# Optimization experiments

Measured on AMD Instinct MI355X. Metric: run time of the kernel, lower is better.

## Reference

```python
import jax, jax.numpy as jnp
import numpy as np

N = 100_000   # nodes (patches)
E = 500_000   # directed edges (kNN, k=5)
F_IN, NHID, GDIM, NCLS = 512, 128, 32, 3
RATIO = 0.2

def _k(n):
    return int(np.ceil(RATIO * n))

K1, K2, K3 = _k(N), _k(_k(N)), _k(_k(_k(N)))


def setup_inputs() -> dict:
    key = jax.random.key(0)
    ks = jax.random.split(key, 20)
    def w(k, shape):
        fan_in = shape[0]
        return jax.random.normal(k, shape, jnp.float32) / np.sqrt(fan_in)
    return {
        "x": jax.random.normal(ks[0], (N, F_IN), jnp.float32),
        "edge_index": jax.random.randint(ks[1], (2, E), 0, N, jnp.int32),
        # SAGEConv1 (lin_l on aggregated msgs w/ bias, lin_r on root w/o bias)
        "w1l": w(ks[2], (F_IN, NHID)), "b1l": jnp.zeros((NHID,), jnp.float32),
        "w1r": w(ks[3], (F_IN, NHID)),
        # SAGPooling1 score GNN = GCNConv(nhid, 1)
        "g1w": w(ks[4], (NHID, 1)), "g1b": jnp.zeros((1,), jnp.float32),
        "w2l": w(ks[5], (NHID, NHID)), "b2l": jnp.zeros((NHID,), jnp.float32),
        "w2r": w(ks[6], (NHID, NHID)),
        "g2w": w(ks[7], (NHID, 1)), "g2b": jnp.zeros((1,), jnp.float32),
        "w3l": w(ks[8], (NHID, NHID)), "b3l": jnp.zeros((NHID,), jnp.float32),
        "w3r": w(ks[9], (NHID, NHID)),
        "g3w": w(ks[10], (NHID, 1)), "g3b": jnp.zeros((1,), jnp.float32),
        "lw1": w(ks[11], (2 * NHID, NHID)), "lb1": jnp.zeros((NHID,), jnp.float32),
        "lw2": w(ks[12], (NHID, GDIM)), "lb2": jnp.zeros((GDIM,), jnp.float32),
        "lw3": w(ks[13], (GDIM, NCLS)), "lb3": jnp.zeros((NCLS,), jnp.float32),
    }


def sage_conv(x, src, dst, ev, Wl, bl, Wr, n):
    """PyG SAGEConv: lin_l(mean_{j->i} x_j) + lin_r(x_i); ev is float edge-valid mask."""
    msg = x[src] * ev[:, None]                      # [E, F] gather
    agg = jax.ops.segment_sum(msg, dst, num_segments=n)
    cnt = jax.ops.segment_sum(ev, dst, num_segments=n)
    mean = agg / jnp.maximum(cnt, 1.0)[:, None]
    return mean @ Wl + bl + x @ Wr


def gcn_score(x, src, dst, ev, W, b, n):
    """GCNConv(nhid,1) with self-loops and symmetric norm -> per-node score [n]."""
    xw = x @ W                                       # [n, 1]
    deg = jax.ops.segment_sum(ev, dst, num_segments=n) + 1.0  # self-loop
    dis = jax.lax.rsqrt(deg)
    norm = dis[src] * dis[dst] * ev                  # [E]
    agg = jax.ops.segment_sum(xw[src] * norm[:, None], dst, num_segments=n)
    agg = agg + xw * (dis * dis)[:, None]            # self-loop term
    return (agg + b)[:, 0]


def sag_pool(x, src, dst, ev, W, b, n, k):
    """SAGPooling: top-k by GCN score, x' = x[perm] * tanh(score[perm]); relabel/mask edges."""
    score = gcn_score(x, src, dst, ev, W, b, n)
    topv, perm = jax.lax.top_k(score, k)
    xk = x[perm] * jnp.tanh(topv)[:, None]
    rank = jnp.full((n,), -1, jnp.int32).at[perm].set(jnp.arange(k, dtype=jnp.int32))
    ns, nd = rank[src], rank[dst]
    nev = ev * ((ns >= 0) & (nd >= 0)).astype(x.dtype)
    return xk, jnp.maximum(ns, 0), jnp.maximum(nd, 0), nev


def reference(x, edge_index, w1l, b1l, w1r, g1w, g1b, w2l, b2l, w2r, g2w, g2b,
              w3l, b3l, w3r, g3w, g3b, lw1, lb1, lw2, lb2, lw3, lb3):
    src, dst = edge_index[0], edge_index[1]
    ev = jnp.ones((src.shape[0],), x.dtype)

    h = jax.nn.relu(sage_conv(x, src, dst, ev, w1l, b1l, w1r, N))
    h, src, dst, ev = sag_pool(h, src, dst, ev, g1w, g1b, N, K1)
    x1 = jnp.concatenate([h.max(axis=0), h.mean(axis=0)])[None]   # [1, 2*nhid]

    h = jax.nn.relu(sage_conv(h, src, dst, ev, w2l, b2l, w2r, K1))
    h, src, dst, ev = sag_pool(h, src, dst, ev, g2w, g2b, K1, K2)
    x2 = jnp.concatenate([h.max(axis=0), h.mean(axis=0)])[None]

    h = jax.nn.relu(sage_conv(h, src, dst, ev, w3l, b3l, w3r, K2))
    h, src, dst, ev = sag_pool(h, src, dst, ev, g3w, g3b, K2, K3)
    x3 = jnp.concatenate([h.max(axis=0), h.mean(axis=0)])[None]

    g = x1 + x2 + x3
    g = jax.nn.relu(g @ lw1 + lb1)          # dropout is identity in eval
    features = jax.nn.relu(g @ lw2 + lb2)   # [1, grph_dim]
    out = features @ lw3 + lb3              # [1, num_classes], act=None
    return features, out
```

## Files before the change

### kernel.cpp

```cpp
#include <hip/hip_runtime.h>
#include <hip/hip_bf16.h>
#include <cstdint>
#include <cstddef>

#define N_NODES 100000
#define N_EDGES 500000
#define F_IN    512
#define NHID    128
#define KP1     20000
#define KP2     4000
#define KP3     800
#define GDIM    32
#define NCLS    3
#define HISTB   128
#define RDB     64
#define RELB    768

typedef __attribute__((ext_vector_type(8))) short bf16x8;
typedef __attribute__((ext_vector_type(4))) float f32x4;

static __device__ __forceinline__ unsigned enc_f(float f) {
  unsigned u = __float_as_uint(f);
  return (u & 0x80000000u) ? ~u : (u | 0x80000000u);
}
static __device__ __forceinline__ float dec_f(unsigned u) {
  unsigned v = (u & 0x80000000u) ? (u & 0x7FFFFFFFu) : ~u;
  return __uint_as_float(v);
}
static __device__ __forceinline__ unsigned short f2bf(float f) {
  unsigned u = __float_as_uint(f);
  return (unsigned short)((u + 0x7FFFu + ((u >> 16) & 1u)) >> 16);
}
static __device__ __forceinline__ unsigned pk2(float a, float b) {
  return (unsigned)f2bf(a) | ((unsigned)f2bf(b) << 16);
}
static __device__ __forceinline__ float bf2f(unsigned short v) {
  return __uint_as_float(((unsigned)v) << 16);
}

static __device__ __forceinline__ void hist_tail(int hb, int t, int nthreads,
                                                 const int* __restrict__ dst,
                                                 const int* __restrict__ ev,
                                                 int* __restrict__ cnt) {
  for (int e = hb * nthreads + t; e < N_EDGES; e += HISTB * nthreads) {
    if (ev && !ev[e]) continue;
    atomicAdd(cnt + dst[e], 1);
  }
}

__global__ __launch_bounds__(256) void wt_prep(const float* __restrict__ w1l,
                                               const float* __restrict__ w1r,
                                               const float* __restrict__ w2l,
                                               const float* __restrict__ w2r,
                                               const float* __restrict__ w3l,
                                               const float* __restrict__ w3r,
                                               unsigned short* __restrict__ Wt,
                                               unsigned short* __restrict__ Wt2,
                                               unsigned short* __restrict__ Wt3,
                                               int* __restrict__ cnt0,
                                               unsigned* __restrict__ hist) {
  __shared__ unsigned short T[128][130];
  int blk = blockIdx.x;
  int t = threadIdx.x;
  if (blk == 0) hist[t] = 0u;
  for (int i = blk * 256 + t; i < N_NODES; i += (int)gridDim.x * 256) cnt0[i] = 0;

  const float* W;
  unsigned short* Wo;
  int mat, k0, KW;
  if (blk < 8) {
    mat = blk >> 2; k0 = (blk & 3) * 128; KW = 512;
    W = mat ? w1r : w1l; Wo = Wt;
  } else if (blk < 10) {
    mat = blk - 8; k0 = 0; KW = 128;
    W = mat ? w2r : w2l; Wo = Wt2;
  } else {
    mat = blk - 10; k0 = 0; KW = 128;
    W = mat ? w3r : w3l; Wo = Wt3;
  }
  for (int q = 0; q < 64; ++q) {
    int idx = q * 256 + t;
    int r = idx >> 7, c = idx & 127;
    T[r][c] = f2bf(W[(size_t)(k0 + r) * 128 + c]);
  }
  __syncthreads();
  int nn = t & 127;
  int kc = (t >> 7) * 64;
  for (int j8 = 0; j8 < 8; ++j8) {
    uint4 w;
    int kb = kc + j8 * 8;
    w.x = (unsigned)T[kb + 0][nn] | ((unsigned)T[kb + 1][nn] << 16);
    w.y = (unsigned)T[kb + 2][nn] | ((unsigned)T[kb + 3][nn] << 16);
    w.z = (unsigned)T[kb + 4][nn] | ((unsigned)T[kb + 5][nn] << 16);
    w.w = (unsigned)T[kb + 6][nn] | ((unsigned)T[kb + 7][nn] << 16);
    *reinterpret_cast<uint4*>(Wo + ((size_t)(mat * 128 + nn) * KW + k0 + kb)) = w;
  }
}

__global__ __launch_bounds__(512) void gemm_mfma(const void* __restrict__ Ain, int aBf16,
                                                 const unsigned short* __restrict__ Wt,
                                                 unsigned short* __restrict__ O1b,
                                                 unsigned short* __restrict__ Gb,
                                                 int n, int K, int nbA,
                                                 const int* __restrict__ edst,
                                                 const int* __restrict__ eev,
                                                 int* __restrict__ cnt,
                                                 const unsigned short* __restrict__ Hprev,
                                                 int kprev,
                                                 unsigned* __restrict__ maxaccP,
                                                 float* __restrict__ sumaccP) {
  __shared__ unsigned short Alds[128 * 64];
  __shared__ float red[4][128];
  const int t = threadIdx.x;
  if ((int)blockIdx.x >= nbA + HISTB) {
    int hb = blockIdx.x - nbA - HISTB;
    int f = t & 127, rg = t >> 7;
    float m = -INFINITY, s = 0.f;
    for (int r = hb * 4 + rg; r < kprev; r += RDB * 4) {
      float v = bf2f(Hprev[(size_t)r * 128 + f]);
      m = fmaxf(m, v); s += v;
    }
    red[rg][f] = m;
    __syncthreads();
    if (t < 128) {
      float mm = fmaxf(fmaxf(red[0][t], red[1][t]), fmaxf(red[2][t], red[3][t]));
      atomicMax(maxaccP + t, enc_f(mm));
    }
    __syncthreads();
    red[rg][f] = s;
    __syncthreads();
    if (t < 128) {
      float ss = red[0][t] + red[1][t] + red[2][t] + red[3][t];
      atomicAdd(sumaccP + t, ss);
    }
    return;
  }
  if ((int)blockIdx.x >= nbA) {
    hist_tail(blockIdx.x - nbA, t, 512, edst, eev, cnt);
    return;
  }
  const int wave = t >> 6;
  const int lane = t & 63;
  const int wr = wave >> 2;
  const int wc = wave & 3;
  const int l15 = lane & 15, l4 = lane >> 4;
  const int bm = blockIdx.x * 128;
  f32x4 zero = {0.f, 0.f, 0.f, 0.f};
  f32x4 acc[4][4];
#pragma unroll
  for (int i = 0; i < 4; ++i)
#pragma unroll
    for (int j = 0; j < 4; ++j) acc[i][j] = zero;

  const int sr = t >> 2;
  const int skc = (t & 3) * 16;
  const int sgr = bm + sr;
  const float* apf = (const float*)Ain + (size_t)sgr * K + skc;
  const unsigned short* apb = (const unsigned short*)Ain + (size_t)sgr * K + skc;
  const unsigned sbase = sr * 128 + skc * 2;
  const unsigned ssw = (sr & 7) << 4;

  for (int k0 = 0; k0 < K; k0 += 64) {
    __syncthreads();
    if (aBf16) {
      uint4 w0 = make_uint4(0u, 0u, 0u, 0u), w1 = make_uint4(0u, 0u, 0u, 0u);
      if (sgr < n) {
        w0 = *reinterpret_cast<const uint4*>(apb + k0);
        w1 = *reinterpret_cast<const uint4*>(apb + k0 + 8);
      }
      *reinterpret_cast<uint4*>((char*)Alds + (sbase ^ ssw)) = w0;
      *reinterpret_cast<uint4*>((char*)Alds + ((sbase + 16) ^ ssw)) = w1;
    } else {
      float4 v0, v1, v2, v3;
      if (sgr < n) {
        v0 = *reinterpret_cast<const float4*>(apf + k0);
        v1 = *reinterpret_cast<const float4*>(apf + k0 + 4);
        v2 = *reinterpret_cast<const float4*>(apf + k0 + 8);
        v3 = *reinterpret_cast<const float4*>(apf + k0 + 12);
      } else {
        v0 = v1 = v2 = v3 = make_float4(0.f, 0.f, 0.f, 0.f);
      }
      uint4 w0, w1;
      w0.x = pk2(v0.x, v0.y); w0.y = pk2(v0.z, v0.w);
      w0.z = pk2(v1.x, v1.y); w0.w = pk2(v1.z, v1.w);
      w1.x = pk2(v2.x, v2.y); w1.y = pk2(v2.z, v2.w);
      w1.z = pk2(v3.x, v3.y); w1.w = pk2(v3.z, v3.w);
      *reinterpret_cast<uint4*>((char*)Alds + (sbase ^ ssw)) = w0;
      *reinterpret_cast<uint4*>((char*)Alds + ((sbase + 16) ^ ssw)) = w1;
    }
    __syncthreads();
#pragma unroll
    for (int kk = 0; kk < 2; ++kk) {
      bf16x8 af[4], bfr[4];
#pragma unroll
      for (int fr = 0; fr < 4; ++fr) {
        int row = wr * 64 + fr * 16 + l15;
        unsigned ba = (unsigned)(row * 128 + kk * 64 + l4 * 16) ^ ((unsigned)(row & 7) << 4);
        af[fr] = *reinterpret_cast<const bf16x8*>((const char*)Alds + ba);
      }
#pragma unroll
      for (int fn = 0; fn < 4; ++fn) {
        int col = wc * 64 + fn * 16 + l15;
        bfr[fn] = *reinterpret_cast<const bf16x8*>(Wt + ((size_t)col * K + k0 + kk * 32 + l4 * 8));
      }
#pragma unroll
      for (int fr = 0; fr < 4; ++fr)
#pragma unroll
        for (int fn = 0; fn < 4; ++fn)
          acc[fr][fn] = __builtin_amdgcn_mfma_f32_16x16x32_bf16(af[fr], bfr[fn], acc[fr][fn], 0, 0, 0);
    }
  }

#pragma unroll
  for (int fr = 0; fr < 4; ++fr) {
#pragma unroll
    for (int fn = 0; fn < 4; ++fn) {
      int colg = wc * 64 + fn * 16 + l15;
      int col = colg & 127;
      int row0 = bm + wr * 64 + fr * 16 + l4 * 4;
#pragma unroll
      for (int r2 = 0; r2 < 4; ++r2) {
        int gr = row0 + r2;
        if (gr < n) {
          unsigned short bv = f2bf(acc[fr][fn][r2]);
          if (colg < 128) O1b[(size_t)gr * 128 + col] = bv;
          else            Gb [(size_t)gr * 128 + col] = bv;
        }
      }
    }
  }
}

__global__ void scan1(const int* __restrict__ cnt, int n,
                      int* __restrict__ incl, int* __restrict__ bsum) {
  __shared__ int sh[256];
  int t = threadIdx.x, i = blockIdx.x * 256 + t;
  int v = (i < n) ? cnt[i] : 0;
  sh[t] = v; __syncthreads();
  for (int o = 1; o < 256; o <<= 1) {
    int a = (t >= o) ? sh[t - o] : 0;
    __syncthreads(); sh[t] += a; __syncthreads();
  }
  if (i < n) incl[i] = sh[t];
  if (t == 255) bsum[blockIdx.x] = sh[255];
}

__global__ void scan2(int* __restrict__ bsum, int nb) {
  __shared__ int sh[512];
  int t = threadIdx.x;
  int v = (t < nb) ? bsum[t] : 0;
  sh[t] = v; __syncthreads();
  for (int o = 1; o < 512; o <<= 1) {
    int a = (t >= o) ? sh[t - o] : 0;
    __syncthreads(); sh[t] += a; __syncthreads();
  }
  if (t < nb) bsum[t] = sh[t] - v;
}

__global__ void scan3(const int* __restrict__ cnt, const int* __restrict__ incl,
                      const int* __restrict__ bsum, int n,
                      int* __restrict__ rowstart, int* __restrict__ ptr,
                      int* __restrict__ cnt_next, int n_next) {
  int i = blockIdx.x * 256 + threadIdx.x;
  if (i < n_next) cnt_next[i] = 0;
  if (i >= n) return;
  int excl = incl[i] - cnt[i] + bsum[blockIdx.x];
  rowstart[i] = excl; ptr[i] = excl;
  if (i == n - 1) rowstart[n] = excl + cnt[i];
}

__global__ __launch_bounds__(1024) void csr_scan_one(const int* __restrict__ cnt, int n,
                                                     int* __restrict__ rowstart,
                                                     int* __restrict__ ptr,
                                                     int* __restrict__ cnt_next, int n_next) {
  __shared__ int sg[1024];
  const int t = threadIdx.x;
  for (int i = t; i < n_next; i += 1024) cnt_next[i] = 0;
  const int chunk = (n + 1023) >> 10;
  const int i0 = t * chunk;
  const int i1 = (i0 + chunk < n) ? i0 + chunk : n;
  int c = 0;
  for (int i = i0; i < i1; ++i) c += cnt[i];
  sg[t] = c;
  __syncthreads();
  for (int o = 1; o < 1024; o <<= 1) {
    int a = (t >= o) ? sg[t - o] : 0;
    __syncthreads();
    sg[t] += a;
    __syncthreads();
  }
  int excl = sg[t] - c;
  for (int i = i0; i < i1; ++i) {
    rowstart[i] = excl; ptr[i] = excl;
    excl += cnt[i];
  }
  if (t == 1023) rowstart[n] = sg[1023];
}

__global__ void scatter_csr(const int* __restrict__ src, const int* __restrict__ dst,
                            const int* __restrict__ ev, int* __restrict__ ptr,
                            int* __restrict__ csr_src) {
  int e = blockIdx.x * 256 + threadIdx.x;
  if (e >= N_EDGES) return;
  if (ev && !ev[e]) return;
  int p = atomicAdd(ptr + dst[e], 1);
  csr_src[p] = src[e];
}

__global__ void segsort(const int* __restrict__ rowstart, int* __restrict__ csr, int n) {
  int i = blockIdx.x * 256 + threadIdx.x;
  if (i >= n) return;
  int b = rowstart[i], e = rowstart[i + 1];
  for (int j = b + 1; j < e; ++j) {
    int v = csr[j], k = j - 1;
    while (k >= b && csr[k] > v) { csr[k + 1] = csr[k]; --k; }
    csr[k + 1] = v;
  }
}

__global__ void agg_fin(const unsigned short* __restrict__ X1b, const int* __restrict__ rowstart,
                        const int* __restrict__ csr, const float* __restrict__ bias,
                        const float* __restrict__ gw,
                        unsigned short* __restrict__ Gb, float* __restrict__ xw, int n) {
  int wid = (blockIdx.x * 256 + threadIdx.x) >> 6;
  if (wid >= n) return;
  int lane = threadIdx.x & 63;
  int b = rowstart[wid], e = rowstart[wid + 1];
  float sx = 0.f, sy = 0.f;
  int p = b;
  for (; p + 3 < e; p += 4) {
    int s0 = csr[p], s1 = csr[p + 1], s2 = csr[p + 2], s3 = csr[p + 3];
    unsigned v0 = *reinterpret_cast<const unsigned*>(X1b + (size_t)s0 * 128 + lane * 2);
    unsigned v1 = *reinterpret_cast<const unsigned*>(X1b + (size_t)s1 * 128 + lane * 2);
    unsigned v2 = *reinterpret_cast<const unsigned*>(X1b + (size_t)s2 * 128 + lane * 2);
    unsigned v3 = *reinterpret_cast<const unsigned*>(X1b + (size_t)s3 * 128 + lane * 2);
    sx += bf2f((unsigned short)(v0 & 0xFFFFu)); sy += bf2f((unsigned short)(v0 >> 16));
    sx += bf2f((unsigned short)(v1 & 0xFFFFu)); sy += bf2f((unsigned short)(v1 >> 16));
    sx += bf2f((unsigned short)(v2 & 0xFFFFu)); sy += bf2f((unsigned short)(v2 >> 16));
    sx += bf2f((unsigned short)(v3 & 0xFFFFu)); sy += bf2f((unsigned short)(v3 >> 16));
  }
  for (; p < e; ++p) {
    int s0 = csr[p];
    unsigned v0 = *reinterpret_cast<const unsigned*>(X1b + (size_t)s0 * 128 + lane * 2);
    sx += bf2f((unsigned short)(v0 & 0xFFFFu));
    sy += bf2f((unsigned short)(v0 >> 16));
  }
  int c = e - b; if (c < 1) c = 1;
  float inv = 1.f / (float)c;
  float2 bi = *reinterpret_cast<const float2*>(bias + lane * 2);
  unsigned gv = *reinterpret_cast<const unsigned*>(Gb + (size_t)wid * 128 + lane * 2);
  float gx = bf2f((unsigned short)(gv & 0xFFFFu));
  float gy = bf2f((unsigned short)(gv >> 16));
  float2 o = make_float2(fmaxf(sx * inv + bi.x + gx, 0.f),
                         fmaxf(sy * inv + bi.y + gy, 0.f));
  *reinterpret_cast<unsigned*>(Gb + (size_t)wid * 128 + lane * 2) = pk2(o.x, o.y);
  float2 gwv = *reinterpret_cast<const float2*>(gw + lane * 2);
  float s = o.x * gwv.x + o.y * gwv.y;
  for (int off = 32; off; off >>= 1) s += __shfl_down(s, off);
  if (lane == 0) xw[wid] = s;
}

__global__ void gcn_score_csr(const float* __restrict__ xw, const int* __restrict__ rowstart,
                              const int* __restrict__ csr, const int* __restrict__ cnt,
                              const float* __restrict__ gb,
                              float* __restrict__ score, unsigned* __restrict__ keys, int n,
                              unsigned* __restrict__ state, int kout) {
  int i = blockIdx.x * 256 + threadIdx.x;
  if (i == 0) { state[0] = 0u; state[1] = (unsigned)kout; }
  if (i >= n) return;
  int b = rowstart[i], e = rowstart[i + 1];
  float di = rsqrtf((float)(e - b) + 1.f);
  float s = 0.f;
  int p = b;
  for (; p + 3 < e; p += 4) {
    int s0 = csr[p], s1 = csr[p + 1], s2 = csr[p + 2], s3 = csr[p + 3];
    float x0 = xw[s0], x1 = xw[s1], x2 = xw[s2], x3 = xw[s3];
    float c0 = (float)cnt[s0], c1 = (float)cnt[s1];
    float c2 = (float)cnt[s2], c3 = (float)cnt[s3];
    s += x0 * rsqrtf(c0 + 1.f);
    s += x1 * rsqrtf(c1 + 1.f);
    s += x2 * rsqrtf(c2 + 1.f);
    s += x3 * rsqrtf(c3 + 1.f);
  }
  for (; p < e; ++p) {
    int s0 = csr[p];
    s += xw[s0] * rsqrtf((float)cnt[s0] + 1.f);
  }
  float sc = s * di + xw[i] * di * di + gb[0];
  score[i] = sc;
  keys[i] = enc_f(sc);
}

__global__ void topk_hist(const unsigned* __restrict__ keys, int n,
                          const unsigned* __restrict__ state, unsigned mask, int shift,
                          unsigned* __restrict__ hist) {
  __shared__ unsigned h[256];
  int t = threadIdx.x;
  h[t] = 0u;
  __syncthreads();
  unsigned pref = state[0];
  for (int i = blockIdx.x * 256 + t; i < n; i += gridDim.x * 256) {
    unsigned k = keys[i];
    if ((k & mask) == pref) atomicAdd(&h[(k >> shift) & 0xFFu], 1u);
  }
  __syncthreads();
  unsigned hv = h[t];
  if (hv) atomicAdd(&hist[t], hv);
}

__global__ void topk_pick(unsigned* state, unsigned* hist, int shift) {
  __shared__ unsigned h[256], a[256];
  int t = threadIdx.x;
  unsigned hv = hist[t];
  hist[t] = 0;
  h[t] = hv;
  __syncthreads();
  a[t] = h[255 - t];
  __syncthreads();
  for (int o = 1; o < 256; o <<= 1) {
    unsigned v = (t >= o) ? a[t - o] : 0u;
    __syncthreads();
    a[t] += v;
    __syncthreads();
  }
  unsigned krem = state[1];
  unsigned Sb  = a[255 - t];
  unsigned Sb1 = (t == 255) ? 0u : a[255 - (t + 1)];
  if (Sb >= krem && Sb1 < krem) {
    state[0] |= ((unsigned)t) << shift;
    state[1] = krem - Sb1;
  }
}

__global__ void scanA(const unsigned* __restrict__ keys, int n,
                      const unsigned* __restrict__ state,
                      unsigned* __restrict__ pgt, unsigned* __restrict__ peq) {
  __shared__ unsigned sg[256], se[256];
  int t = threadIdx.x;
  int i = blockIdx.x * 256 + t;
  unsigned kth = state[0];
  unsigned g = 0, e = 0;
  if (i < n) { unsigned k = keys[i]; g = (k > kth); e = (k == kth); }
  sg[t] = g; se[t] = e;
  __syncthreads();
  for (int s = 128; s; s >>= 1) {
    if (t < s) { sg[t] += sg[t + s]; se[t] += se[t + s]; }
    __syncthreads();
  }
  if (t == 0) { pgt[blockIdx.x] = sg[0]; peq[blockIdx.x] = se[0]; }
}

__global__ void scanB(unsigned* pgt, unsigned* peq, int nb,
                      unsigned* __restrict__ maxacc, float* __restrict__ sumacc) {
  __shared__ unsigned a[512], b[512];
  int t = threadIdx.x;
  if (t < 128) { maxacc[t] = 0u; sumacc[t] = 0.f; }
  unsigned og = (t < nb) ? pgt[t] : 0u;
  unsigned oe = (t < nb) ? peq[t] : 0u;
  a[t] = og; b[t] = oe;
  __syncthreads();
  for (int o = 1; o < 512; o <<= 1) {
    unsigned av = (t >= o) ? a[t - o] : 0u;
    unsigned bv = (t >= o) ? b[t - o] : 0u;
    __syncthreads();
    a[t] += av; b[t] += bv;
    __syncthreads();
  }
  if (t < nb) { pgt[t] = a[t] - og; peq[t] = b[t] - oe; }
}

__global__ void scanC(const unsigned* __restrict__ keys, int n,
                      const unsigned* __restrict__ state,
                      const unsigned* __restrict__ pgt, const unsigned* __restrict__ peq,
                      int K, int* __restrict__ rank) {
  __shared__ unsigned sg[256], se[256];
  int t = threadIdx.x;
  int i = blockIdx.x * 256 + t;
  unsigned kth = state[0], krem = state[1];
  unsigned g = 0, e = 0;
  if (i < n) { unsigned k = keys[i]; g = (k > kth); e = (k == kth); }
  sg[t] = g; se[t] = e;
  __syncthreads();
  for (int o = 1; o < 256; o <<= 1) {
    unsigned av = (t >= o) ? sg[t - o] : 0u;
    unsigned bv = (t >= o) ? se[t - o] : 0u;
    __syncthreads();
    sg[t] += av; se[t] += bv;
    __syncthreads();
  }
  if (i < n) {
    int r = -1;
    unsigned n_gt = (unsigned)K - krem;
    if (g) r = (int)(pgt[blockIdx.x] + sg[t] - 1);
    else if (e) {
      unsigned pe = peq[blockIdx.x] + se[t] - 1;
      if (pe < krem) r = (int)(n_gt + pe);
    }
    rank[i] = r;
  }
}

__global__ __launch_bounds__(1024) void select_one(const unsigned* __restrict__ keys, int n,
                                                   int K, int* __restrict__ rank,
                                                   unsigned* __restrict__ maxacc,
                                                   float* __restrict__ sumacc) {
  __shared__ unsigned h[256], a[256];
  __shared__ unsigned sg[1024], se[1024];
  __shared__ unsigned s_pref, s_krem;
  const int t = threadIdx.x;
  if (t < 128) { maxacc[t] = 0u; sumacc[t] = 0.f; }
  if (t == 0) { s_pref = 0u; s_krem = (unsigned)K; }
  __syncthreads();

#pragma unroll
  for (int p = 0; p < 4; ++p) {
    const int shift = 24 - 8 * p;
    const unsigned mask = (p == 0) ? 0u : (0xFFFFFFFFu << (shift + 8));
    if (t < 256) h[t] = 0u;
    __syncthreads();
    unsigned pref = s_pref;
    for (int i = t; i < n; i += 1024) {
      unsigned k = keys[i];
      if ((k & mask) == pref) atomicAdd(&h[(k >> shift) & 0xFFu], 1u);
    }
    __syncthreads();
    if (t < 256) a[t] = h[255 - t];
    __syncthreads();
    for (int o = 1; o < 256; o <<= 1) {
      unsigned v = (t >= o && t < 256) ? a[t - o] : 0u;
      __syncthreads();
      if (t < 256) a[t] += v;
      __syncthreads();
    }
    unsigned krem = s_krem;
    __syncthreads();
    if (t < 256) {
      unsigned Sb  = a[255 - t];
      unsigned Sb1 = (t == 255) ? 0u : a[255 - (t + 1)];
      if (Sb >= krem && Sb1 < krem) {
        s_pref |= ((unsigned)t) << shift;
        s_krem = krem - Sb1;
      }
    }
    __syncthreads();
  }

  const unsigned kth = s_pref;
  const unsigned krem = s_krem;
  const unsigned n_gt = (unsigned)K - krem;
  const int chunk = (n + 1023) >> 10;
  const int i0 = t * chunk;
  const int i1 = (i0 + chunk < n) ? i0 + chunk : n;
  unsigned cg = 0, ce = 0;
  for (int i = i0; i < i1; ++i) {
    unsigned k = keys[i];
    cg += (k > kth); ce += (k == kth);
  }
  sg[t] = cg; se[t] = ce;
  __syncthreads();
  for (int o = 1; o < 1024; o <<= 1) {
    unsigned ag = (t >= o) ? sg[t - o] : 0u;
    unsigned ae = (t >= o) ? se[t - o] : 0u;
    __syncthreads();
    sg[t] += ag; se[t] += ae;
    __syncthreads();
  }
  unsigned rg = sg[t] - cg;
  unsigned re = se[t] - ce;
  for (int i = i0; i < i1; ++i) {
    unsigned k = keys[i];
    int r = -1;
    if (k > kth) {
      r = (int)(rg++);
    } else if (k == kth) {
      unsigned pe = re++;
      if (pe < krem) r = (int)(n_gt + pe);
    }
    rank[i] = r;
  }
}

__global__ void pool_rel(const unsigned short* __restrict__ Gb, const float* __restrict__ score,
                         const int* __restrict__ rank, unsigned short* __restrict__ Houtb, int n,
                         int nbP, int mode,
                         const int* __restrict__ ei,
                         int* __restrict__ src2, int* __restrict__ dst2,
                         int* __restrict__ ev2) {
  const int t = threadIdx.x;
  if ((int)blockIdx.x >= nbP) {
    int hb = blockIdx.x - nbP;
    if (mode == 0) {
      for (int e = hb * 256 + t; e < N_EDGES; e += RELB * 256) {
        int s = ei[e], d = ei[N_EDGES + e];
        int rs = rank[s], rd = rank[d];
        int valid = (rs >= 0) & (rd >= 0);
        src2[e] = rs > 0 ? rs : 0;
        dst2[e] = rd > 0 ? rd : 0;
        ev2[e] = valid;
      }
    } else if (mode == 1) {
      for (int e = hb * 256 + t; e < N_EDGES; e += RELB * 256) {
        if (!ev2[e]) continue;
        int s = src2[e], d = dst2[e];
        int rs = rank[s], rd = rank[d];
        int valid = (rs >= 0) & (rd >= 0);
        src2[e] = rs > 0 ? rs : 0;
        dst2[e] = rd > 0 ? rd : 0;
        ev2[e] = valid;
      }
    }
    return;
  }
  int gid = blockIdx.x * 256 + t;
  int i = gid >> 5;
  if (i >= n) return;
  int r = rank[i];
  if (r < 0) return;
  int q = gid & 31;
  float tv = tanhf(score[i]);
  uint2 v = *reinterpret_cast<const uint2*>(Gb + (size_t)i * 128 + q * 4);
  float a0 = bf2f((unsigned short)(v.x & 0xFFFFu)) * tv;
  float a1 = bf2f((unsigned short)(v.x >> 16)) * tv;
  float a2 = bf2f((unsigned short)(v.y & 0xFFFFu)) * tv;
  float a3 = bf2f((unsigned short)(v.y >> 16)) * tv;
  uint2 o = make_uint2(pk2(a0, a1), pk2(a2, a3));
  *reinterpret_cast<uint2*>(Houtb + (size_t)r * 128 + q * 4) = o;
}

__global__ void readout_reduce(const unsigned short* __restrict__ Hb, int k,
                               unsigned* __restrict__ maxacc, float* __restrict__ sumacc) {
  int f = threadIdx.x;
  float m = -INFINITY, s = 0.f;
  for (int r = blockIdx.x; r < k; r += gridDim.x) {
    float v = bf2f(Hb[(size_t)r * 128 + f]);
    m = fmaxf(m, v);
    s += v;
  }
  atomicMax(maxacc + f, enc_f(m));
  atomicAdd(sumacc + f, s);
}

__global__ void head_kernel(const unsigned* __restrict__ maxacc3,
                            const float* __restrict__ sumacc3,
                            const float* __restrict__ lw1, const float* __restrict__ lb1,
                            const float* __restrict__ lw2, const float* __restrict__ lb2,
                            const float* __restrict__ lw3, const float* __restrict__ lb3,
                            float* __restrict__ out) {
  __shared__ float g[256];
  __shared__ float t1[128];
  __shared__ float t2[32];
  int t = threadIdx.x;
  float v;
  if (t < 128) {
    v = dec_f(maxacc3[t]) + dec_f(maxacc3[128 + t]) + dec_f(maxacc3[256 + t]);
  } else {
    int f = t - 128;
    v = sumacc3[f] * (1.f / (float)KP1) + sumacc3[128 + f] * (1.f / (float)KP2) +
        sumacc3[256 + f] * (1.f / (float)KP3);
  }
  g[t] = v;
  __syncthreads();
  if (t < 128) {
    float s = lb1[t];
    for (int j = 0; j < 256; ++j) s += g[j] * lw1[j * 128 + t];
    t1[t] = fmaxf(s, 0.f);
  }
  __syncthreads();
  if (t < 32) {
    float s = lb2[t];
    for (int j = 0; j < 128; ++j) s += t1[j] * lw2[j * 32 + t];
    float v2 = fmaxf(s, 0.f);
    t2[t] = v2;
    out[t] = v2;
  }
  __syncthreads();
  if (t < NCLS) {
    float s = lb3[t];
    for (int j = 0; j < 32; ++j) s += t2[j] * lw3[j * 3 + t];
    out[32 + t] = s;
  }
}

extern "C" void kernel_launch(void* const* d_in, const int* in_sizes, int n_in_,
                              void* d_out, int out_size, void* d_ws, size_t ws_size,
                              hipStream_t stream) {
  (void)in_sizes; (void)n_in_; (void)out_size; (void)ws_size;
  const float* x   = (const float*)d_in[0];
  const int*   ei  = (const int*)d_in[1];
  const float* w1l = (const float*)d_in[2];
  const float* b1l = (const float*)d_in[3];
  const float* w1r = (const float*)d_in[4];
  const float* g1w = (const float*)d_in[5];
  const float* g1b = (const float*)d_in[6];
  const float* w2l = (const float*)d_in[7];
  const float* b2l = (const float*)d_in[8];
  const float* w2r = (const float*)d_in[9];
  const float* g2w = (const float*)d_in[10];
  const float* g2b = (const float*)d_in[11];
  const float* w3l = (const float*)d_in[12];
  const float* b3l = (const float*)d_in[13];
  const float* w3r = (const float*)d_in[14];
  const float* g3w = (const float*)d_in[15];
  const float* g3b = (const float*)d_in[16];
  const float* lw1 = (const float*)d_in[17];
  const float* lb1 = (const float*)d_in[18];
  const float* lw2 = (const float*)d_in[19];
  const float* lb2 = (const float*)d_in[20];
  const float* lw3 = (const float*)d_in[21];
  const float* lb3 = (const float*)d_in[22];
  float* out = (float*)d_out;

  char* base = (char*)d_ws;
  size_t off = 0;
  auto alloc = [&](size_t bytes) {
    void* p = base + off;
    off = (off + bytes + 255) & ~(size_t)255;
    return p;
  };
  unsigned short* X1b = (unsigned short*)alloc((size_t)N_NODES * 128 * 2);
  unsigned short* Gb  = (unsigned short*)alloc((size_t)N_NODES * 128 * 2);
  unsigned short* H2b = (unsigned short*)alloc((size_t)KP1 * 128 * 2);
  unsigned short* H3b = (unsigned short*)alloc((size_t)KP2 * 128 * 2);
  unsigned short* H4b = (unsigned short*)alloc((size_t)KP3 * 128 * 2);
  int*      cntA   = (int*)alloc((size_t)N_NODES * 4);
  int*      cntB   = (int*)alloc((size_t)KP1 * 4);
  int*      incl   = (int*)alloc((size_t)N_NODES * 4);
  int*      bsum   = (int*)alloc(512 * 4);
  int*      rowstart = (int*)alloc((size_t)(N_NODES + 1) * 4);
  int*      ptr    = (int*)alloc((size_t)N_NODES * 4);
  int*      csr    = (int*)alloc((size_t)N_EDGES * 4);
  float*    xw     = (float*)alloc((size_t)N_NODES * 4);
  float*    score  = (float*)alloc((size_t)N_NODES * 4);
  unsigned* keys   = (unsigned*)alloc((size_t)N_NODES * 4);
  int*      rank   = (int*)alloc((size_t)N_NODES * 4);
  int*      src2   = (int*)alloc((size_t)N_EDGES * 4);
  int*      dst2   = (int*)alloc((size_t)N_EDGES * 4);
  int*      ev2    = (int*)alloc((size_t)N_EDGES * 4);
  unsigned* pgt    = (unsigned*)alloc(512 * 4);
  unsigned* peq    = (unsigned*)alloc(512 * 4);
  unsigned* hist   = (unsigned*)alloc(256 * 4);
  unsigned* state  = (unsigned*)alloc(64);
  unsigned* maxacc3 = (unsigned*)alloc(3 * 128 * 4);
  float*    sumacc3 = (float*)alloc(3 * 128 * 4);
  unsigned short* Wt  = (unsigned short*)alloc((size_t)256 * 512 * 2);
  unsigned short* Wt2 = (unsigned short*)alloc((size_t)256 * 128 * 2);
  unsigned short* Wt3 = (unsigned short*)alloc((size_t)256 * 128 * 2);

  struct Layer {
    const void* H; int n; int K; int kout;
    const float *bl, *gw, *gb;
    const unsigned short* Wt;
    unsigned short* Hout;
    int* cnt;
    int* cnt_next;
    int n_next;
  };
  Layer L[3] = {
    { x,   N_NODES, F_IN, KP1, b1l, g1w, g1b, Wt,  H2b, cntA, cntB, KP1 },
    { H2b, KP1,     NHID, KP2, b2l, g2w, g2b, Wt2, H3b, cntB, cntA, KP2 },
    { H3b, KP2,     NHID, KP3, b3l, g3w, g3b, Wt3, H4b, cntA, nullptr, 0 },
  };

  wt_prep<<<12, 256, 0, stream>>>(w1l, w1r, w2l, w2r, w3l, w3r, Wt, Wt2, Wt3, cntA, hist);

  for (int l = 0; l < 3; ++l) {
    const Layer& P = L[l];
    const int n = P.n;
    const int nb = (n + 255) / 256;
    const bool small = (n <= 4000);
    const int* esrc = (l == 0) ? ei            : src2;
    const int* edst = (l == 0) ? ei + N_EDGES  : dst2;
    const int* eev  = (l == 0) ? (const int*)nullptr : ev2;

    {
      int nbA = (n + 127) / 128;
      int grid = nbA + HISTB + (l > 0 ? RDB : 0);
      gemm_mfma<<<dim3(grid), 512, 0, stream>>>(
          P.H, (l > 0) ? 1 : 0, P.Wt, X1b, Gb, n, P.K, nbA, edst, eev, P.cnt,
          (l > 0) ? L[l - 1].Hout : (const unsigned short*)nullptr,
          (l > 0) ? L[l - 1].kout : 0,
          maxacc3 + (l > 0 ? (l - 1) : 0) * 128,
          sumacc3 + (l > 0 ? (l - 1) : 0) * 128);
    }

    if (small) {
      csr_scan_one<<<1, 1024, 0, stream>>>(P.cnt, n, rowstart, ptr, P.cnt_next, P.n_next);
    } else {
      scan1<<<nb, 256, 0, stream>>>(P.cnt, n, incl, bsum);
      scan2<<<1, 512, 0, stream>>>(bsum, nb);
      scan3<<<nb, 256, 0, stream>>>(P.cnt, incl, bsum, n, rowstart, ptr, P.cnt_next, P.n_next);
    }
    scatter_csr<<<(N_EDGES + 255) / 256, 256, 0, stream>>>(esrc, edst, eev, ptr, csr);
    segsort<<<nb, 256, 0, stream>>>(rowstart, csr, n);

    agg_fin<<<(n * 64 + 255) / 256, 256, 0, stream>>>(X1b, rowstart, csr, P.bl, P.gw, Gb, xw, n);

    gcn_score_csr<<<nb, 256, 0, stream>>>(xw, rowstart, csr, P.cnt, P.gb, score, keys, n,
                                          state, P.kout);

    if (small) {
      select_one<<<1, 1024, 0, stream>>>(keys, n, P.kout, rank,
                                         maxacc3 + l * 128, sumacc3 + l * 128);
    } else {
      int hb = nb < 256 ? nb : 256;
      for (int p = 0; p < 4; ++p) {
        int shift = 24 - 8 * p;
        unsigned mask = (p == 0) ? 0u : (0xFFFFFFFFu << (shift + 8));
        topk_hist<<<hb, 256, 0, stream>>>(keys, n, state, mask, shift, hist);
        topk_pick<<<1, 256, 0, stream>>>(state, hist, shift);
      }
      scanA<<<nb, 256, 0, stream>>>(keys, n, state, pgt, peq);
      scanB<<<1, 512, 0, stream>>>(pgt, peq, nb, maxacc3 + l * 128, sumacc3 + l * 128);
      scanC<<<nb, 256, 0, stream>>>(keys, n, state, pgt, peq, P.kout, rank);
    }

    int mode = (l == 0) ? 0 : (l == 1 ? 1 : 2);
    int nbP = (n * 32 + 255) / 256;
    int grid = nbP + (mode < 2 ? RELB : 0);
    pool_rel<<<grid, 256, 0, stream>>>(Gb, score, rank, P.Hout, n, nbP, mode,
                                       ei, src2, dst2, ev2);
  }

  readout_reduce<<<64, 128, 0, stream>>>(H4b, KP3, maxacc3 + 2 * 128, sumacc3 + 2 * 128);
  head_kernel<<<1, 256, 0, stream>>>(maxacc3, sumacc3, lw1, lb1, lw2, lb2, lw3, lb3, out);
}
```

Measured before the change: 415.5 us.

## Drop LDS staging in GEMM; each wave owns 16 rows across all 256 columns

The MFMA GEMM no longer stages the A tile through shared memory with block-wide barriers. Each of the 8 waves now loads its own 16 rows of A directly from global memory into registers and computes all 16 column fragments with 16 accumulators. This removes LDS traffic and the __syncthreads per k-step. In exchange, each wave reads the full weight matrix, so B-fragment loads rise about fourfold per block. It also keeps 16 accumulator vectors live, which increases register pressure.

```diff
diff --git a/kernel.cpp b/kernel.cpp
--- a/kernel.cpp
+++ b/kernel.cpp
@@ -109,7 +109,6 @@
                                                  int kprev,
                                                  unsigned* __restrict__ maxaccP,
                                                  float* __restrict__ sumaccP) {
-  __shared__ unsigned short Alds[128 * 64];
   __shared__ float red[4][128];
   const int t = threadIdx.x;
   if ((int)blockIdx.x >= nbA + HISTB) {
@@ -139,93 +138,62 @@
     hist_tail(blockIdx.x - nbA, t, 512, edst, eev, cnt);
     return;
   }
-  const int wave = t >> 6;
+  const int wg = t >> 6;
   const int lane = t & 63;
-  const int wr = wave >> 2;
-  const int wc = wave & 3;
   const int l15 = lane & 15, l4 = lane >> 4;
   const int bm = blockIdx.x * 128;
+  const int row = bm + wg * 16 + l15;
+  const bool rv = row < n;
+
   f32x4 zero = {0.f, 0.f, 0.f, 0.f};
-  f32x4 acc[4][4];
+  f32x4 acc[16];
 #pragma unroll
-  for (int i = 0; i < 4; ++i)
-#pragma unroll
-    for (int j = 0; j < 4; ++j) acc[i][j] = zero;
-
-  const int sr = t >> 2;
-  const int skc = (t & 3) * 16;
-  const int sgr = bm + sr;
-  const float* apf = (const float*)Ain + (size_t)sgr * K + skc;
-  const unsigned short* apb = (const unsigned short*)Ain + (size_t)sgr * K + skc;
-  const unsigned sbase = sr * 128 + skc * 2;
-  const unsigned ssw = (sr & 7) << 4;
+  for (int i = 0; i < 16; ++i) acc[i] = zero;
+
+  const float* apf = (const float*)Ain + (size_t)row * K;
+  const unsigned short* apb = (const unsigned short*)Ain + (size_t)row * K;
 
   for (int k0 = 0; k0 < K; k0 += 64) {
-    __syncthreads();
-    if (aBf16) {
-      uint4 w0 = make_uint4(0u, 0u, 0u, 0u), w1 = make_uint4(0u, 0u, 0u, 0u);
-      if (sgr < n) {
-        w0 = *reinterpret_cast<const uint4*>(apb + k0);
-        w1 = *reinterpret_cast<const uint4*>(apb + k0 + 8);
-      }
-      *reinterpret_cast<uint4*>((char*)Alds + (sbase ^ ssw)) = w0;
-      *reinterpret_cast<uint4*>((char*)Alds + ((sbase + 16) ^ ssw)) = w1;
-    } else {
-      float4 v0, v1, v2, v3;
-      if (sgr < n) {
-        v0 = *reinterpret_cast<const float4*>(apf + k0);
-        v1 = *reinterpret_cast<const float4*>(apf + k0 + 4);
-        v2 = *reinterpret_cast<const float4*>(apf + k0 + 8);
-        v3 = *reinterpret_cast<const float4*>(apf + k0 + 12);
-      } else {
-        v0 = v1 = v2 = v3 = make_float4(0.f, 0.f, 0.f, 0.f);
-      }
-      uint4 w0, w1;
-      w0.x = pk2(v0.x, v0.y); w0.y = pk2(v0.z, v0.w);
-      w0.z = pk2(v1.x, v1.y); w0.w = pk2(v1.z, v1.w);
-      w1.x = pk2(v2.x, v2.y); w1.y = pk2(v2.z, v2.w);
-      w1.z = pk2(v3.x, v3.y); w1.w = pk2(v3.z, v3.w);
-      *reinterpret_cast<uint4*>((char*)Alds + (sbase ^ ssw)) = w0;
-      *reinterpret_cast<uint4*>((char*)Alds + ((sbase + 16) ^ ssw)) = w1;
-    }
-    __syncthreads();
 #pragma unroll
     for (int kk = 0; kk < 2; ++kk) {
-      bf16x8 af[4], bfr[4];
-#pragma unroll
-      for (int fr = 0; fr < 4; ++fr) {
-        int row = wr * 64 + fr * 16 + l15;
-        unsigned ba = (unsigned)(row * 128 + kk * 64 + l4 * 16) ^ ((unsigned)(row & 7) << 4);
-        af[fr] = *reinterpret_cast<const bf16x8*>((const char*)Alds + ba);
+      const int kb = k0 + kk * 32 + l4 * 8;
+      bf16x8 af;
+      if (aBf16) {
+        uint4 w = make_uint4(0u, 0u, 0u, 0u);
+        if (rv) w = *reinterpret_cast<const uint4*>(apb + kb);
+        af = *reinterpret_cast<const bf16x8*>(&w);
+      } else {
+        float4 v0 = make_float4(0.f, 0.f, 0.f, 0.f), v1 = v0;
+        if (rv) {
+          v0 = *reinterpret_cast<const float4*>(apf + kb);
+          v1 = *reinterpret_cast<const float4*>(apf + kb + 4);
+        }
+        uint4 w;
+        w.x = pk2(v0.x, v0.y); w.y = pk2(v0.z, v0.w);
+        w.z = pk2(v1.x, v1.y); w.w = pk2(v1.z, v1.w);
+        af = *reinterpret_cast<const bf16x8*>(&w);
       }
 #pragma unroll
-      for (int fn = 0; fn < 4; ++fn) {
-        int col = wc * 64 + fn * 16 + l15;
-        bfr[fn] = *reinterpret_cast<const bf16x8*>(Wt + ((size_t)col * K + k0 + kk * 32 + l4 * 8));
+      for (int fn = 0; fn < 16; ++fn) {
+        int col = fn * 16 + l15;
+        bf16x8 bfr = *reinterpret_cast<const bf16x8*>(Wt + ((size_t)col * K + kb));
+        acc[fn] = __builtin_amdgcn_mfma_f32_16x16x32_bf16(af, bfr, acc[fn], 0, 0, 0);
       }
+    }
+  }
+
 #pragma unroll
-      for (int fr = 0; fr < 4; ++fr)
+  for (int fn = 0; fn < 16; ++fn) {
+    int colg = fn * 16 + l15;
+    int col = colg & 127;
+    int row0 = bm + wg * 16 + l4 * 4;
 #pragma unroll
-        for (int fn = 0; fn < 4; ++fn)
-          acc[fr][fn] = __builtin_amdgcn_mfma_f32_16x16x32_bf16(af[fr], bfr[fn], acc[fr][fn], 0, 0, 0);
-    }
-  }
-
-#pragma unroll
-  for (int fr = 0; fr < 4; ++fr) {
-#pragma unroll
-    for (int fn = 0; fn < 4; ++fn) {
-      int colg = wc * 64 + fn * 16 + l15;
-      int col = colg & 127;
-      int row0 = bm + wr * 64 + fr * 16 + l4 * 4;
-#pragma unroll
-      for (int r2 = 0; r2 < 4; ++r2) {
-        int gr = row0 + r2;
-        if (gr < n) {
-          unsigned short bv = f2bf(acc[fr][fn][r2]);
-          if (colg < 128) O1b[(size_t)gr * 128 + col] = bv;
-          else            Gb [(size_t)gr * 128 + col] = bv;
-        }
+    for (int r2 = 0; r2 < 4; ++r2) {
+      int gr = row0 + r2;
+      if (gr < n) {
+        unsigned short bv = f2bf(acc[fn][r2]);
+        if (colg < 128) O1b[(size_t)gr * 128 + col] = bv;
+        else            Gb [(size_t)gr * 128 + col] = bv;
       }
     }
   }
```

Result: slower. 594.0 us (+43.0%).
